# Kernel tuning notes

Hardware: AMD Instinct MI355X
Metric: run time of the kernel (lower is better)

## Reference

```python
import jax, jax.numpy as jnp
import numpy as np

IN_C = 128
OUT_C = 128
N = 100000
E = 1600000


def spmm(row, col, w, x, n):
    # out[i] = sum_{e: row[e]==i} w[e] * x[col[e]]  (sparse adjacency matmul)
    return jax.ops.segment_sum(w[:, None] * x[col], row, num_segments=n)


def setup_inputs() -> dict:
    key = jax.random.key(0)
    ks = jax.random.split(key, 10)
    x = jax.random.normal(ks[0], (N, IN_C), dtype=jnp.float32)
    row = jax.random.randint(ks[1], (E,), 0, N, dtype=jnp.int32)
    col = jax.random.randint(ks[2], (E,), 0, N, dtype=jnp.int32)
    edge_weight = jax.random.uniform(ks[3], (E,), dtype=jnp.float32)
    s = 1.0 / np.sqrt(IN_C)
    W0 = jax.random.uniform(ks[4], (IN_C, OUT_C), minval=-s, maxval=s, dtype=jnp.float32)
    b0 = jax.random.uniform(ks[5], (OUT_C,), minval=-s, maxval=s, dtype=jnp.float32)
    W1 = jax.random.uniform(ks[6], (IN_C, OUT_C), minval=-s, maxval=s, dtype=jnp.float32)
    b1 = jax.random.uniform(ks[7], (OUT_C,), minval=-s, maxval=s, dtype=jnp.float32)
    W2 = jax.random.uniform(ks[8], (IN_C, OUT_C), minval=-s, maxval=s, dtype=jnp.float32)
    b2 = jax.random.uniform(ks[9], (OUT_C,), minval=-s, maxval=s, dtype=jnp.float32)
    return {"x": x, "row": row, "col": col, "edge_weight": edge_weight,
            "W0": W0, "b0": b0, "W1": W1, "b1": b1, "W2": W2, "b2": b2}


def reference(x, row, col, edge_weight, W0, b0, W1, b1, W2, b2):
    n = x.shape[0]
    # hop 0: plain linear
    x0 = x @ W0 + b0
    # hop 1: linear then one SpMM propagation
    x1 = spmm(row, col, edge_weight, x @ W1 + b1, n)
    # hop 2: linear then two SpMM propagations
    x2 = spmm(row, col, edge_weight,
              spmm(row, col, edge_weight, x @ W2 + b2, n), n)
    return jnp.concatenate([x0, x1, x2], axis=1)  # [N, 3*OUT_C]
```

## Files before the change

kernel.cpp:

```cpp
#include <hip/hip_runtime.h>

typedef __attribute__((ext_vector_type(8))) short bf16x8;
typedef __attribute__((ext_vector_type(4))) float f32x4;
typedef __attribute__((ext_vector_type(2))) float f32x2;
typedef __attribute__((ext_vector_type(2))) uint u32x2;
typedef __attribute__((ext_vector_type(4))) uint u32x4;

static inline size_t align256(size_t x) { return (x + 255) & ~size_t(255); }

__device__ inline ushort f2bf(float f) {
  uint u = __float_as_uint(f);
  return (ushort)((u + 0x7FFFu + ((u >> 16) & 1u)) >> 16);
}
__device__ inline float bf2f(ushort h) { return __uint_as_float(((uint)h) << 16); }


__device__ inline uint fp8x4_enc(float a0, float a1, float a2, float a3) {
#if __has_builtin(__builtin_amdgcn_cvt_pk_fp8_f32)
  int v = 0;
  v = __builtin_amdgcn_cvt_pk_fp8_f32(a0, a1, v, false);
  v = __builtin_amdgcn_cvt_pk_fp8_f32(a2, a3, v, true);
  return (uint)v;
#else
  float a[4] = {a0, a1, a2, a3};
  uint r = 0;
#pragma unroll
  for (int k = 0; k < 4; ++k) {
    uint u = __float_as_uint(a[k]);
    uint s = (u >> 24) & 0x80u;
    uint au = u & 0x7FFFFFFFu;
    uint b;
    if (au < 0x3C800000u) {
      b = s;
    } else {
      uint rr = au + 0x7FFFFu + ((au >> 20) & 1u);
      uint e = (rr >> 23) - 120u;
      uint m = (rr >> 20) & 7u;
      b = s | (e << 3) | m;
    }
    r |= b << (8 * k);
  }
  return r;
#endif
}

__device__ inline f32x4 fp8x4_dec(uint u) {
  f32x4 r;
#if __has_builtin(__builtin_amdgcn_cvt_pk_f32_fp8)
  auto lo = __builtin_amdgcn_cvt_pk_f32_fp8((int)u, false);
  auto hi = __builtin_amdgcn_cvt_pk_f32_fp8((int)u, true);
  r[0] = lo[0]; r[1] = lo[1]; r[2] = hi[0]; r[3] = hi[1];
#else
#pragma unroll
  for (int k = 0; k < 4; ++k) {
    uint b = (u >> (8 * k)) & 0xFFu;
    uint f = ((b & 0x80u) << 24) | (((b & 0x7Fu) + (120u << 3)) << 20);
    r[k] = (b & 0x7Fu) ? __uint_as_float(f) : 0.f;
  }
#endif
  return r;
}

__device__ inline float ew_dec(uint u) { return __uint_as_float((u & 0x7FFFu) << 16); }

#define BW_SHIFT 7
#define NBUCK_MAX 1024
#define NCHUNK 256
#define PREP_BLOCKS 96


__global__ __launch_bounds__(512) void build_a_kernel(
    const int* __restrict__ row, int* __restrict__ bcnt,
    int* __restrict__ chunk_hist, int E, int chunk,
    const float* __restrict__ W0, const float* __restrict__ W1,
    const float* __restrict__ W2, ushort* __restrict__ Wt,
    int* __restrict__ done, int* __restrict__ boff, int* __restrict__ gcur,
    int* __restrict__ offp, int n) {
  __shared__ int h[NBUCK_MAX];
  int bid = blockIdx.x;
  int t = threadIdx.x;
  if (bid < NCHUNK) {
    for (int i = t; i < NBUCK_MAX; i += 512) h[i] = 0;
    __syncthreads();
    int c0 = bid * chunk, c1 = min(c0 + chunk, E);
    for (int i = c0 + t; i < c1; i += 512)
      atomicAdd(&h[row[i] >> BW_SHIFT], 1);
    __syncthreads();
    for (int i = t; i < NBUCK_MAX; i += 512) {
      int c = h[i];
      chunk_hist[bid * NBUCK_MAX + i] = c;
      if (c) atomicAdd(&bcnt[i], c);
    }
  } else {
    int i = (bid - NCHUNK) * 512 + t;
    int mat = i >> 14, r = i & 16383;
    int k = r >> 7, c = r & 127;
    const float* W = (mat == 0) ? W0 : (mat == 1) ? W1 : W2;
    Wt[mat * 16384 + c * 128 + k] = f2bf(W[k * 128 + c]);
  }
  __shared__ int ticket;
  __syncthreads();
  if (t == 0) {
    __threadfence();
    ticket = atomicAdd(done, 1);
  }
  __syncthreads();
  if (ticket == (int)gridDim.x - 1) {
    __threadfence();
    int v0 = bcnt[2 * t], v1 = bcnt[2 * t + 1];
    int pair = v0 + v1;
    h[t] = pair;
    __syncthreads();
    for (int o = 1; o < 512; o <<= 1) {
      int a = (t >= o) ? h[t - o] : 0;
      __syncthreads();
      h[t] += a;
      __syncthreads();
    }
    int excl = h[t] - pair;
    boff[2 * t] = excl;          gcur[2 * t] = excl;
    boff[2 * t + 1] = excl + v0; gcur[2 * t + 1] = excl + v0;
    if (t == 511) boff[NBUCK_MAX] = E;
    if (t == 0) offp[n] = E;
  }
}


__global__ __launch_bounds__(512) void bin_scatter(
    const int* __restrict__ row, const int* __restrict__ col,
    const float* __restrict__ w, int* __restrict__ gcur,
    const int* __restrict__ chunk_hist, int2* __restrict__ es_tmp,
    int E, int chunk) {
  __shared__ int lbase[NBUCK_MAX];
  __shared__ int lh[NBUCK_MAX];
  int bid = blockIdx.x;
  int t = threadIdx.x;
  for (int i = t; i < NBUCK_MAX; i += 512) {
    int c = chunk_hist[bid * NBUCK_MAX + i];
    lbase[i] = c ? atomicAdd(&gcur[i], c) : 0;
    lh[i] = 0;
  }
  __syncthreads();
  int c0 = bid * chunk, c1 = min(c0 + chunk, E);
  for (int i = c0 + t; i < c1; i += 512) {
    int r = row[i];
    int b = r >> BW_SHIFT;
    int pos = lbase[b] + atomicAdd(&lh[b], 1);
    es_tmp[pos] = make_int2(((r & 127) << 17) | col[i], __float_as_int(w[i]));
  }
}


__global__ __launch_bounds__(256) void sort_gemm_kernel(
    const int2* __restrict__ es_tmp, const int* __restrict__ boff,
    uint* __restrict__ es, int* __restrict__ offp, int ng,
    const float* __restrict__ x, const ushort* __restrict__ Wt,
    const float* __restrict__ b0, const float* __restrict__ b1,
    const float* __restrict__ b2,
    float* __restrict__ out0, unsigned char* __restrict__ y12, int n) {
  int t = threadIdx.x;
  if ((int)blockIdx.x >= ng) {
    __shared__ int lh[128];
    __shared__ int lex[128];
    int b = (int)blockIdx.x - ng;
    int base = boff[b], cnt = boff[b + 1] - base;
    if (t < 128) lh[t] = 0;
    __syncthreads();
    for (int i = t; i < cnt; i += 256)
      atomicAdd(&lh[(es_tmp[base + i].x >> 17) & 127], 1);
    __syncthreads();
    if (t < 128) lex[t] = lh[t];
    __syncthreads();
    for (int o = 1; o < 128; o <<= 1) {
      int a = (t >= o && t < 128) ? lex[t - o] : 0;
      __syncthreads();
      if (t < 128) lex[t] += a;
      __syncthreads();
    }
    if (t < 128) {
      int v = lh[t];
      int excl = lex[t] - v;
      int node = (b << BW_SHIFT) + t;
      if (node < n) offp[node] = base + excl;
      lh[t] = excl;
    }
    __syncthreads();
    for (int i = t; i < cnt; i += 256) {
      int2 ed = es_tmp[base + i];
      int nl = (ed.x >> 17) & 127;
      int pos = base + atomicAdd(&lh[nl], 1);
      uint wb = (uint)f2bf(__int_as_float(ed.y)) & 0x7FFFu;
      es[pos] = ((uint)(ed.x & 0x1FFFF) << 15) | wb;
    }
    return;
  }
  int w = t >> 6;
  int l = t & 63;
  int lr = l & 15;
  int lg = l >> 4;
  int rows0 = (int)blockIdx.x * 256 + w * 64;

  bf16x8 xf[4][4];
#pragma unroll
  for (int rt = 0; rt < 4; ++rt) {
    int row = rows0 + rt * 16 + lr;
    bool ok = row < n;
    const float* base = x + (size_t)row * 128;
#pragma unroll
    for (int kc = 0; kc < 4; ++kc) {
      float4 a = ok ? *(const float4*)(base + kc * 32 + lg * 8) : make_float4(0, 0, 0, 0);
      float4 c = ok ? *(const float4*)(base + kc * 32 + lg * 8 + 4) : make_float4(0, 0, 0, 0);
      bf16x8 f;
      f[0] = (short)f2bf(a.x); f[1] = (short)f2bf(a.y);
      f[2] = (short)f2bf(a.z); f[3] = (short)f2bf(a.w);
      f[4] = (short)f2bf(c.x); f[5] = (short)f2bf(c.y);
      f[6] = (short)f2bf(c.z); f[7] = (short)f2bf(c.w);
      xf[rt][kc] = f;
    }
  }

  for (int mat = 0; mat < 3; ++mat) {
    const ushort* Wm = Wt + mat * 16384;
    const float* bias = (mat == 0) ? b0 : (mat == 1) ? b1 : b2;
#pragma unroll 1
    for (int ct = 0; ct < 8; ++ct) {
      bf16x8 wf[4];
#pragma unroll
      for (int kc = 0; kc < 4; ++kc)
        wf[kc] = *(const bf16x8*)(Wm + (ct * 16 + lr) * 128 + kc * 32 + lg * 8);
      float4 bb = *(const float4*)(bias + ct * 16 + lg * 4);
      f32x4 acc[4];
#pragma unroll
      for (int rt = 0; rt < 4; ++rt) {
        acc[rt][0] = bb.x; acc[rt][1] = bb.y; acc[rt][2] = bb.z; acc[rt][3] = bb.w;
      }
#pragma unroll
      for (int kc = 0; kc < 4; ++kc)
#pragma unroll
        for (int rt = 0; rt < 4; ++rt)
          acc[rt] = __builtin_amdgcn_mfma_f32_16x16x32_bf16(wf[kc], xf[rt][kc], acc[rt], 0, 0, 0);
#pragma unroll
      for (int rt = 0; rt < 4; ++rt) {
        int row = rows0 + rt * 16 + lr;
        if (row >= n) continue;
        int col = ct * 16 + lg * 4;
        if (mat == 0) {
          __builtin_nontemporal_store(acc[rt], (f32x4*)(out0 + (size_t)row * 384 + col));
        } else {
          uint v8 = fp8x4_enc(acc[rt][0], acc[rt][1], acc[rt][2], acc[rt][3]);
          unsigned char* Y = y12 + (size_t)row * 256 + ((mat == 2) ? 128 : 0) + col;
          *(uint*)Y = v8;
        }
      }
    }
  }
}


__global__ __launch_bounds__(256) void spmm_dual_kernel(
    const unsigned char* __restrict__ y12,
    float* __restrict__ o1,
    ushort* __restrict__ z2,
    const int* __restrict__ off, const uint* __restrict__ es, int n) {
  int node = blockIdx.x * 8 + ((threadIdx.x >> 6) << 1) + ((threadIdx.x & 63) >> 5);
  if (node >= n) return;
  int h = threadIdx.x & 31;
  int s = off[node], e = off[node + 1];
  float a0 = 0.f, a1 = 0.f, a2 = 0.f, a3 = 0.f;
  float a4 = 0.f, a5 = 0.f, a6 = 0.f, a7 = 0.f;
  int i = s;
  for (; i + 4 <= e; i += 4) {
    u32x2 u[4];
    float w[4];
#pragma unroll
    for (int j = 0; j < 4; ++j) {
      uint ed = es[i + j];
      w[j] = ew_dec(ed);
      u[j] = *(const u32x2*)(y12 + (size_t)(ed >> 15) * 256 + h * 8);
    }
#pragma unroll
    for (int j = 0; j < 4; ++j) {
      f32x4 p = fp8x4_dec(u[j].x), q = fp8x4_dec(u[j].y);
      a0 += w[j] * p[0]; a1 += w[j] * p[1]; a2 += w[j] * p[2]; a3 += w[j] * p[3];
      a4 += w[j] * q[0]; a5 += w[j] * q[1]; a6 += w[j] * q[2]; a7 += w[j] * q[3];
    }
  }
  for (; i < e; ++i) {
    uint ed = es[i];
    float w = ew_dec(ed);
    u32x2 u = *(const u32x2*)(y12 + (size_t)(ed >> 15) * 256 + h * 8);
    f32x4 p = fp8x4_dec(u.x), q = fp8x4_dec(u.y);
    a0 += w * p[0]; a1 += w * p[1]; a2 += w * p[2]; a3 += w * p[3];
    a4 += w * q[0]; a5 += w * q[1]; a6 += w * q[2]; a7 += w * q[3];
  }
  if (h < 16) {
    float* dst = o1 + (size_t)node * 384 + h * 8;
    f32x4 lo; lo[0] = a0; lo[1] = a1; lo[2] = a2; lo[3] = a3;
    f32x4 hi; hi[0] = a4; hi[1] = a5; hi[2] = a6; hi[3] = a7;
    __builtin_nontemporal_store(lo, (f32x4*)dst);
    __builtin_nontemporal_store(hi, (f32x4*)(dst + 4));
  } else {
    u32x4 z;
    z.x = (uint)f2bf(a0) | ((uint)f2bf(a1) << 16);
    z.y = (uint)f2bf(a2) | ((uint)f2bf(a3) << 16);
    z.z = (uint)f2bf(a4) | ((uint)f2bf(a5) << 16);
    z.w = (uint)f2bf(a6) | ((uint)f2bf(a7) << 16);
    *(u32x4*)(z2 + (size_t)node * 128 + (h - 16) * 8) = z;
  }
}


__global__ __launch_bounds__(256) void spmm_single_kernel(
    const ushort* __restrict__ z2,
    float* __restrict__ o2,
    const int* __restrict__ off, const uint* __restrict__ es, int n) {
  int node = blockIdx.x * 8 + ((threadIdx.x >> 6) << 1) + ((threadIdx.x & 63) >> 5);
  if (node >= n) return;
  int h = threadIdx.x & 31;
  int s = off[node], e = off[node + 1];
  float a0 = 0.f, a1 = 0.f, a2 = 0.f, a3 = 0.f;
  int i = s;
  for (; i + 4 <= e; i += 4) {
    u32x2 u[4];
    float w[4];
#pragma unroll
    for (int j = 0; j < 4; ++j) {
      uint ed = es[i + j];
      w[j] = ew_dec(ed);
      u[j] = *(const u32x2*)(z2 + (size_t)(ed >> 15) * 128 + h * 4);
    }
#pragma unroll
    for (int j = 0; j < 4; ++j) {
      a0 += w[j] * bf2f((ushort)u[j].x); a1 += w[j] * bf2f((ushort)(u[j].x >> 16));
      a2 += w[j] * bf2f((ushort)u[j].y); a3 += w[j] * bf2f((ushort)(u[j].y >> 16));
    }
  }
  for (; i < e; ++i) {
    uint ed = es[i];
    float w = ew_dec(ed);
    u32x2 u = *(const u32x2*)(z2 + (size_t)(ed >> 15) * 128 + h * 4);
    a0 += w * bf2f((ushort)u.x); a1 += w * bf2f((ushort)(u.x >> 16));
    a2 += w * bf2f((ushort)u.y); a3 += w * bf2f((ushort)(u.y >> 16));
  }
  f32x4 v; v[0] = a0; v[1] = a1; v[2] = a2; v[3] = a3;
  __builtin_nontemporal_store(v, (f32x4*)(o2 + (size_t)node * 384 + h * 4));
}


extern "C" void kernel_launch(void* const* d_in, const int* in_sizes, int n_in,
                              void* d_out, int out_size, void* d_ws, size_t ws_size,
                              hipStream_t stream) {
  const float* x   = (const float*)d_in[0];
  const int*   row = (const int*)d_in[1];
  const int*   col = (const int*)d_in[2];
  const float* ew  = (const float*)d_in[3];
  const float* W0  = (const float*)d_in[4];
  const float* b0  = (const float*)d_in[5];
  const float* W1  = (const float*)d_in[6];
  const float* b1  = (const float*)d_in[7];
  const float* W2  = (const float*)d_in[8];
  const float* b2  = (const float*)d_in[9];
  float* out = (float*)d_out;

  int n = in_sizes[0] / 128;
  int E = in_sizes[1];

  char* p = (char*)d_ws;
  size_t o = 0;
  unsigned char* y12 = (unsigned char*)(p + o); o = align256(o + (size_t)n * 256);
  ushort* z2  = (ushort*)(p + o); o = align256(o + (size_t)n * 128 * 2);
  ushort* Wt  = (ushort*)(p + o); o = align256(o + (size_t)3 * 16384 * 2);
  int* bcnt   = (int*)(p + o);    o = align256(o + (size_t)(NBUCK_MAX + 1) * 4);
  int* done   = bcnt + NBUCK_MAX;
  int* boff   = (int*)(p + o);    o = align256(o + (size_t)(NBUCK_MAX + 1) * 4);
  int* gcur   = (int*)(p + o);    o = align256(o + (size_t)NBUCK_MAX * 4);
  int* offp   = (int*)(p + o);    o = align256(o + ((size_t)n + 1) * 4);
  int* chist  = (int*)(p + o);    o = align256(o + (size_t)NCHUNK * NBUCK_MAX * 4);
  int2* es_t  = (int2*)(p + o);   o = align256(o + (size_t)E * 8);
  uint* es    = (uint*)(p + o);   o = align256(o + (size_t)E * 4);
  (void)ws_size; (void)n_in; (void)out_size;

  int nbuck = (n + 127) >> 7;
  int ng = (n + 255) / 256;
  int chunk = (E + NCHUNK - 1) / NCHUNK;

  hipMemsetAsync(bcnt, 0, (size_t)(NBUCK_MAX + 1) * 4, stream);

  build_a_kernel<<<NCHUNK + PREP_BLOCKS, 512, 0, stream>>>(
      row, bcnt, chist, E, chunk, W0, W1, W2, Wt, done, boff, gcur, offp, n);

  bin_scatter<<<NCHUNK, 512, 0, stream>>>(row, col, ew, gcur, chist, es_t, E, chunk);

  sort_gemm_kernel<<<ng + nbuck, 256, 0, stream>>>(
      es_t, boff, es, offp, ng,
      x, Wt, b0, b1, b2, out, y12, n);

  spmm_dual_kernel<<<(n + 7) / 8, 256, 0, stream>>>(y12, out + 128, z2,
                                                    offp, es, n);
  spmm_single_kernel<<<(n + 7) / 8, 256, 0, stream>>>(z2, out + 256,
                                                      offp, es, n);
}
```

Before: 226.4 us.

## Propagate raw features before linear transforms using row-sum bias correction

Reorders hop 1 and hop 2 so the first SpMM runs on fp8-quantised raw x (128 columns) instead of the concatenated transformed features (256 columns). The linear layers W1 and W2 are then applied after that propagation, with the bias scaled by each node's weighted degree, which is accumulated in shared memory during the CSR sort. The aim is to halve the gather width of the first SpMM. In exchange it adds an fp8 conversion pass over x, a separate GEMM kernel and an extra bf16 intermediate buffer, and changes where rounding error enters the result.

```diff
diff --git a/kernel.cpp b/kernel.cpp
--- a/kernel.cpp
+++ b/kernel.cpp
@@ -2,7 +2,6 @@
 
 typedef __attribute__((ext_vector_type(8))) short bf16x8;
 typedef __attribute__((ext_vector_type(4))) float f32x4;
-typedef __attribute__((ext_vector_type(2))) float f32x2;
 typedef __attribute__((ext_vector_type(2))) uint u32x2;
 typedef __attribute__((ext_vector_type(4))) uint u32x4;
 
@@ -126,45 +125,59 @@
 }
 
 
-__global__ __launch_bounds__(512) void bin_scatter(
+__global__ __launch_bounds__(512) void scatter_x8_kernel(
     const int* __restrict__ row, const int* __restrict__ col,
     const float* __restrict__ w, int* __restrict__ gcur,
     const int* __restrict__ chunk_hist, int2* __restrict__ es_tmp,
-    int E, int chunk) {
-  __shared__ int lbase[NBUCK_MAX];
-  __shared__ int lh[NBUCK_MAX];
+    int E, int chunk,
+    const float* __restrict__ x, unsigned char* __restrict__ x8, int ne8) {
   int bid = blockIdx.x;
   int t = threadIdx.x;
-  for (int i = t; i < NBUCK_MAX; i += 512) {
-    int c = chunk_hist[bid * NBUCK_MAX + i];
-    lbase[i] = c ? atomicAdd(&gcur[i], c) : 0;
-    lh[i] = 0;
-  }
-  __syncthreads();
-  int c0 = bid * chunk, c1 = min(c0 + chunk, E);
-  for (int i = c0 + t; i < c1; i += 512) {
-    int r = row[i];
-    int b = r >> BW_SHIFT;
-    int pos = lbase[b] + atomicAdd(&lh[b], 1);
-    es_tmp[pos] = make_int2(((r & 127) << 17) | col[i], __float_as_int(w[i]));
-  }
-}
-
-
-__global__ __launch_bounds__(256) void sort_gemm_kernel(
+  if (bid < NCHUNK) {
+    __shared__ int lbase[NBUCK_MAX];
+    __shared__ int lh[NBUCK_MAX];
+    for (int i = t; i < NBUCK_MAX; i += 512) {
+      int c = chunk_hist[bid * NBUCK_MAX + i];
+      lbase[i] = c ? atomicAdd(&gcur[i], c) : 0;
+      lh[i] = 0;
+    }
+    __syncthreads();
+    int c0 = bid * chunk, c1 = min(c0 + chunk, E);
+    for (int i = c0 + t; i < c1; i += 512) {
+      int r = row[i];
+      int b = r >> BW_SHIFT;
+      int pos = lbase[b] + atomicAdd(&lh[b], 1);
+      es_tmp[pos] = make_int2(((r & 127) << 17) | col[i], __float_as_int(w[i]));
+    }
+    return;
+  }
+  int i = (bid - NCHUNK) * 512 + t;
+  if (i < ne8) {
+    size_t base = (size_t)i * 8;
+    float4 a = *(const float4*)(x + base);
+    float4 b = *(const float4*)(x + base + 4);
+    u32x2 v;
+    v.x = fp8x4_enc(a.x, a.y, a.z, a.w);
+    v.y = fp8x4_enc(b.x, b.y, b.z, b.w);
+    *(u32x2*)(x8 + base) = v;
+  }
+}
+
+
+__global__ __launch_bounds__(256) void sort_gemm0_kernel(
     const int2* __restrict__ es_tmp, const int* __restrict__ boff,
-    uint* __restrict__ es, int* __restrict__ offp, int ng,
+    uint* __restrict__ es, int* __restrict__ offp, float* __restrict__ s1,
+    int ng,
     const float* __restrict__ x, const ushort* __restrict__ Wt,
-    const float* __restrict__ b0, const float* __restrict__ b1,
-    const float* __restrict__ b2,
-    float* __restrict__ out0, unsigned char* __restrict__ y12, int n) {
+    const float* __restrict__ b0, float* __restrict__ out0, int n) {
   int t = threadIdx.x;
   if ((int)blockIdx.x >= ng) {
     __shared__ int lh[128];
     __shared__ int lex[128];
+    __shared__ float sld[128];
     int b = (int)blockIdx.x - ng;
     int base = boff[b], cnt = boff[b + 1] - base;
-    if (t < 128) lh[t] = 0;
+    if (t < 128) { lh[t] = 0; sld[t] = 0.f; }
     __syncthreads();
     for (int i = t; i < cnt; i += 256)
       atomicAdd(&lh[(es_tmp[base + i].x >> 17) & 127], 1);
@@ -177,10 +190,9 @@
       if (t < 128) lex[t] += a;
       __syncthreads();
     }
+    int node = (b << BW_SHIFT) + t;
     if (t < 128) {
-      int v = lh[t];
-      int excl = lex[t] - v;
-      int node = (b << BW_SHIFT) + t;
+      int excl = lex[t] - lh[t];
       if (node < n) offp[node] = base + excl;
       lh[t] = excl;
     }
@@ -189,9 +201,13 @@
       int2 ed = es_tmp[base + i];
       int nl = (ed.x >> 17) & 127;
       int pos = base + atomicAdd(&lh[nl], 1);
-      uint wb = (uint)f2bf(__int_as_float(ed.y)) & 0x7FFFu;
+      float wv = __int_as_float(ed.y);
+      atomicAdd(&sld[nl], wv);
+      uint wb = (uint)f2bf(wv) & 0x7FFFu;
       es[pos] = ((uint)(ed.x & 0x1FFFF) << 15) | wb;
     }
+    __syncthreads();
+    if (t < 128 && node < n) s1[node] = sld[t];
     return;
   }
   int w = t >> 6;
@@ -218,99 +234,149 @@
       xf[rt][kc] = f;
     }
   }
-
-  for (int mat = 0; mat < 3; ++mat) {
-    const ushort* Wm = Wt + mat * 16384;
-    const float* bias = (mat == 0) ? b0 : (mat == 1) ? b1 : b2;
 #pragma unroll 1
-    for (int ct = 0; ct < 8; ++ct) {
-      bf16x8 wf[4];
-#pragma unroll
-      for (int kc = 0; kc < 4; ++kc)
-        wf[kc] = *(const bf16x8*)(Wm + (ct * 16 + lr) * 128 + kc * 32 + lg * 8);
-      float4 bb = *(const float4*)(bias + ct * 16 + lg * 4);
-      f32x4 acc[4];
-#pragma unroll
-      for (int rt = 0; rt < 4; ++rt) {
-        acc[rt][0] = bb.x; acc[rt][1] = bb.y; acc[rt][2] = bb.z; acc[rt][3] = bb.w;
+  for (int ct = 0; ct < 8; ++ct) {
+    bf16x8 wf[4];
+#pragma unroll
+    for (int kc = 0; kc < 4; ++kc)
+      wf[kc] = *(const bf16x8*)(Wt + (ct * 16 + lr) * 128 + kc * 32 + lg * 8);
+    float4 bb = *(const float4*)(b0 + ct * 16 + lg * 4);
+    f32x4 acc[4];
+#pragma unroll
+    for (int rt = 0; rt < 4; ++rt) {
+      acc[rt][0] = bb.x; acc[rt][1] = bb.y; acc[rt][2] = bb.z; acc[rt][3] = bb.w;
+    }
+#pragma unroll
+    for (int kc = 0; kc < 4; ++kc)
+#pragma unroll
+      for (int rt = 0; rt < 4; ++rt)
+        acc[rt] = __builtin_amdgcn_mfma_f32_16x16x32_bf16(wf[kc], xf[rt][kc], acc[rt], 0, 0, 0);
+#pragma unroll
+    for (int rt = 0; rt < 4; ++rt) {
+      int row = rows0 + rt * 16 + lr;
+      if (row >= n) continue;
+      int colc = ct * 16 + lg * 4;
+      __builtin_nontemporal_store(acc[rt], (f32x4*)(out0 + (size_t)row * 384 + colc));
+    }
+  }
+}
+
+
+template <bool F32OUT>
+__device__ inline void gemm_p1(const ushort* __restrict__ p1,
+                               const ushort* __restrict__ Wm,
+                               const float* __restrict__ bias,
+                               const float* __restrict__ s1,
+                               int gb, int n, int t,
+                               float* __restrict__ of,
+                               ushort* __restrict__ oh) {
+  int w = t >> 6, l = t & 63, lr = l & 15, lg = l >> 4;
+  int rows0 = gb * 256 + w * 64;
+  bf16x8 zer;
+#pragma unroll
+  for (int q = 0; q < 8; ++q) zer[q] = 0;
+  bf16x8 xf[4][4];
+  float sv[4];
+#pragma unroll
+  for (int rt = 0; rt < 4; ++rt) {
+    int row = rows0 + rt * 16 + lr;
+    bool ok = row < n;
+    sv[rt] = ok ? s1[row] : 0.f;
+    const ushort* base = p1 + (size_t)row * 128;
+#pragma unroll
+    for (int kc = 0; kc < 4; ++kc)
+      xf[rt][kc] = ok ? *(const bf16x8*)(base + kc * 32 + lg * 8) : zer;
+  }
+#pragma unroll 1
+  for (int ct = 0; ct < 8; ++ct) {
+    bf16x8 wf[4];
+#pragma unroll
+    for (int kc = 0; kc < 4; ++kc)
+      wf[kc] = *(const bf16x8*)(Wm + (ct * 16 + lr) * 128 + kc * 32 + lg * 8);
+    float4 bb = *(const float4*)(bias + ct * 16 + lg * 4);
+    f32x4 acc[4];
+#pragma unroll
+    for (int rt = 0; rt < 4; ++rt) {
+      acc[rt][0] = sv[rt] * bb.x; acc[rt][1] = sv[rt] * bb.y;
+      acc[rt][2] = sv[rt] * bb.z; acc[rt][3] = sv[rt] * bb.w;
+    }
+#pragma unroll
+    for (int kc = 0; kc < 4; ++kc)
+#pragma unroll
+      for (int rt = 0; rt < 4; ++rt)
+        acc[rt] = __builtin_amdgcn_mfma_f32_16x16x32_bf16(wf[kc], xf[rt][kc], acc[rt], 0, 0, 0);
+#pragma unroll
+    for (int rt = 0; rt < 4; ++rt) {
+      int row = rows0 + rt * 16 + lr;
+      if (row >= n) continue;
+      int colc = ct * 16 + lg * 4;
+      if (F32OUT) {
+        __builtin_nontemporal_store(acc[rt], (f32x4*)(of + (size_t)row * 384 + colc));
+      } else {
+        u32x2 hh;
+        hh.x = (uint)f2bf(acc[rt][0]) | ((uint)f2bf(acc[rt][1]) << 16);
+        hh.y = (uint)f2bf(acc[rt][2]) | ((uint)f2bf(acc[rt][3]) << 16);
+        *(u32x2*)(oh + (size_t)row * 128 + colc) = hh;
       }
-#pragma unroll
-      for (int kc = 0; kc < 4; ++kc)
-#pragma unroll
-        for (int rt = 0; rt < 4; ++rt)
-          acc[rt] = __builtin_amdgcn_mfma_f32_16x16x32_bf16(wf[kc], xf[rt][kc], acc[rt], 0, 0, 0);
-#pragma unroll
-      for (int rt = 0; rt < 4; ++rt) {
-        int row = rows0 + rt * 16 + lr;
-        if (row >= n) continue;
-        int col = ct * 16 + lg * 4;
-        if (mat == 0) {
-          __builtin_nontemporal_store(acc[rt], (f32x4*)(out0 + (size_t)row * 384 + col));
-        } else {
-          uint v8 = fp8x4_enc(acc[rt][0], acc[rt][1], acc[rt][2], acc[rt][3]);
-          unsigned char* Y = y12 + (size_t)row * 256 + ((mat == 2) ? 128 : 0) + col;
-          *(uint*)Y = v8;
-        }
-      }
-    }
-  }
-}
-
-
-__global__ __launch_bounds__(256) void spmm_dual_kernel(
-    const unsigned char* __restrict__ y12,
-    float* __restrict__ o1,
-    ushort* __restrict__ z2,
+    }
+  }
+}
+
+
+__global__ __launch_bounds__(256) void spmm1_kernel(
+    const unsigned char* __restrict__ x8,
+    ushort* __restrict__ p1,
     const int* __restrict__ off, const uint* __restrict__ es, int n) {
   int node = blockIdx.x * 8 + ((threadIdx.x >> 6) << 1) + ((threadIdx.x & 63) >> 5);
   if (node >= n) return;
   int h = threadIdx.x & 31;
   int s = off[node], e = off[node + 1];
   float a0 = 0.f, a1 = 0.f, a2 = 0.f, a3 = 0.f;
-  float a4 = 0.f, a5 = 0.f, a6 = 0.f, a7 = 0.f;
   int i = s;
-  for (; i + 4 <= e; i += 4) {
-    u32x2 u[4];
-    float w[4];
-#pragma unroll
-    for (int j = 0; j < 4; ++j) {
+  for (; i + 8 <= e; i += 8) {
+    uint u[8];
+    float w[8];
+#pragma unroll
+    for (int j = 0; j < 8; ++j) {
       uint ed = es[i + j];
       w[j] = ew_dec(ed);
-      u[j] = *(const u32x2*)(y12 + (size_t)(ed >> 15) * 256 + h * 8);
-    }
-#pragma unroll
-    for (int j = 0; j < 4; ++j) {
-      f32x4 p = fp8x4_dec(u[j].x), q = fp8x4_dec(u[j].y);
-      a0 += w[j] * p[0]; a1 += w[j] * p[1]; a2 += w[j] * p[2]; a3 += w[j] * p[3];
-      a4 += w[j] * q[0]; a5 += w[j] * q[1]; a6 += w[j] * q[2]; a7 += w[j] * q[3];
+      u[j] = *(const uint*)(x8 + (size_t)(ed >> 15) * 128 + h * 4);
+    }
+#pragma unroll
+    for (int j = 0; j < 8; ++j) {
+      f32x4 p = fp8x4_dec(u[j]);
+      a0 += w[j] * p[0]; a1 += w[j] * p[1];
+      a2 += w[j] * p[2]; a3 += w[j] * p[3];
     }
   }
   for (; i < e; ++i) {
     uint ed = es[i];
     float w = ew_dec(ed);
-    u32x2 u = *(const u32x2*)(y12 + (size_t)(ed >> 15) * 256 + h * 8);
-    f32x4 p = fp8x4_dec(u.x), q = fp8x4_dec(u.y);
+    f32x4 p = fp8x4_dec(*(const uint*)(x8 + (size_t)(ed >> 15) * 128 + h * 4));
     a0 += w * p[0]; a1 += w * p[1]; a2 += w * p[2]; a3 += w * p[3];
-    a4 += w * q[0]; a5 += w * q[1]; a6 += w * q[2]; a7 += w * q[3];
-  }
-  if (h < 16) {
-    float* dst = o1 + (size_t)node * 384 + h * 8;
-    f32x4 lo; lo[0] = a0; lo[1] = a1; lo[2] = a2; lo[3] = a3;
-    f32x4 hi; hi[0] = a4; hi[1] = a5; hi[2] = a6; hi[3] = a7;
-    __builtin_nontemporal_store(lo, (f32x4*)dst);
-    __builtin_nontemporal_store(hi, (f32x4*)(dst + 4));
-  } else {
-    u32x4 z;
-    z.x = (uint)f2bf(a0) | ((uint)f2bf(a1) << 16);
-    z.y = (uint)f2bf(a2) | ((uint)f2bf(a3) << 16);
-    z.z = (uint)f2bf(a4) | ((uint)f2bf(a5) << 16);
-    z.w = (uint)f2bf(a6) | ((uint)f2bf(a7) << 16);
-    *(u32x4*)(z2 + (size_t)node * 128 + (h - 16) * 8) = z;
-  }
-}
-
-
-__global__ __launch_bounds__(256) void spmm_single_kernel(
+  }
+  u32x2 z;
+  z.x = (uint)f2bf(a0) | ((uint)f2bf(a1) << 16);
+  z.y = (uint)f2bf(a2) | ((uint)f2bf(a3) << 16);
+  *(u32x2*)(p1 + (size_t)node * 128 + h * 4) = z;
+}
+
+
+__global__ __launch_bounds__(256) void gemm_z_kernel(
+    const ushort* __restrict__ p1, const ushort* __restrict__ Wt,
+    const float* __restrict__ b1, const float* __restrict__ b2,
+    const float* __restrict__ s1,
+    float* __restrict__ o1, ushort* __restrict__ z2, int ng, int n) {
+  if ((int)blockIdx.x < ng)
+    gemm_p1<false>(p1, Wt + 2 * 16384, b2, s1, blockIdx.x, n, threadIdx.x,
+                   nullptr, z2);
+  else
+    gemm_p1<true>(p1, Wt + 16384, b1, s1, (int)blockIdx.x - ng, n, threadIdx.x,
+                  o1, nullptr);
+}
+
+
+__global__ __launch_bounds__(256) void spmm2_kernel(
     const ushort* __restrict__ z2,
     float* __restrict__ o2,
     const int* __restrict__ off, const uint* __restrict__ es, int n) {
@@ -367,9 +433,11 @@
 
   char* p = (char*)d_ws;
   size_t o = 0;
-  unsigned char* y12 = (unsigned char*)(p + o); o = align256(o + (size_t)n * 256);
+  unsigned char* x8 = (unsigned char*)(p + o); o = align256(o + (size_t)n * 128);
+  ushort* p1  = (ushort*)(p + o); o = align256(o + (size_t)n * 128 * 2);
   ushort* z2  = (ushort*)(p + o); o = align256(o + (size_t)n * 128 * 2);
   ushort* Wt  = (ushort*)(p + o); o = align256(o + (size_t)3 * 16384 * 2);
+  float* s1   = (float*)(p + o);  o = align256(o + (size_t)n * 4);
   int* bcnt   = (int*)(p + o);    o = align256(o + (size_t)(NBUCK_MAX + 1) * 4);
   int* done   = bcnt + NBUCK_MAX;
   int* boff   = (int*)(p + o);    o = align256(o + (size_t)(NBUCK_MAX + 1) * 4);
@@ -382,21 +450,26 @@
 
   int nbuck = (n + 127) >> 7;
   int ng = (n + 255) / 256;
+  int nsp = (n + 7) / 8;
   int chunk = (E + NCHUNK - 1) / NCHUNK;
+  int ne8 = n * 128 / 8;
+  int xb = (ne8 + 511) / 512;
 
   hipMemsetAsync(bcnt, 0, (size_t)(NBUCK_MAX + 1) * 4, stream);
 
   build_a_kernel<<<NCHUNK + PREP_BLOCKS, 512, 0, stream>>>(
       row, bcnt, chist, E, chunk, W0, W1, W2, Wt, done, boff, gcur, offp, n);
 
-  bin_scatter<<<NCHUNK, 512, 0, stream>>>(row, col, ew, gcur, chist, es_t, E, chunk);
-
-  sort_gemm_kernel<<<ng + nbuck, 256, 0, stream>>>(
-      es_t, boff, es, offp, ng,
-      x, Wt, b0, b1, b2, out, y12, n);
-
-  spmm_dual_kernel<<<(n + 7) / 8, 256, 0, stream>>>(y12, out + 128, z2,
-                                                    offp, es, n);
-  spmm_single_kernel<<<(n + 7) / 8, 256, 0, stream>>>(z2, out + 256,
-                                                      offp, es, n);
-}
+  scatter_x8_kernel<<<NCHUNK + xb, 512, 0, stream>>>(
+      row, col, ew, gcur, chist, es_t, E, chunk, x, x8, ne8);
+
+  sort_gemm0_kernel<<<ng + nbuck, 256, 0, stream>>>(
+      es_t, boff, es, offp, s1, ng, x, Wt, b0, out, n);
+
+  spmm1_kernel<<<nsp, 256, 0, stream>>>(x8, p1, offp, es, n);
+
+  gemm_z_kernel<<<2 * ng, 256, 0, stream>>>(p1, Wt, b1, b2, s1,
+                                            out + 128, z2, ng, n);
+
+  spmm2_kernel<<<nsp, 256, 0, stream>>>(z2, out + 256, offp, es, n);
+}
```

After: 239.2 us. +5.7%, slower.
